# Optimization experiments

Hardware: AMD Instinct MI355X
Metric: run time of the kernel (lower is better)

Reference implementation:

```python
import jax, jax.numpy as jnp
import numpy as np

GRAVITY = 9.81007  # pypose default, gravity vector [0,0,g]

# Quaternions are xyzw (pypose SO3 convention). q1*q2 composes rotations R1@R2.

def qmul(q1, q2):
    v1, w1 = q1[..., :3], q1[..., 3:]
    v2, w2 = q2[..., :3], q2[..., 3:]
    w = w1 * w2 - jnp.sum(v1 * v2, axis=-1, keepdims=True)
    v = w1 * v2 + w2 * v1 + jnp.cross(v1, v2)
    return jnp.concatenate([v, w], axis=-1)

def qinv(q):
    return jnp.concatenate([-q[..., :3], q[..., 3:]], axis=-1)

def qrot(q, v):
    # rotate vector v by unit quaternion q: v + 2*cross(qv, cross(qv,v) + qw*v)
    qv, qw = q[..., :3], q[..., 3:]
    t = jnp.cross(qv, v) + qw * v
    return v + 2.0 * jnp.cross(qv, t)

def so3_exp(phi):
    # so3 -> SO3 quaternion: q = [phi*sin(|phi|/2)/|phi|, cos(|phi|/2)]
    theta = jnp.linalg.norm(phi, axis=-1, keepdims=True)
    small = theta < 1e-6
    safe = jnp.where(small, 1.0, theta)
    k = jnp.where(small, 0.5 - theta * theta / 48.0, jnp.sin(0.5 * theta) / safe)
    return jnp.concatenate([phi * k, jnp.cos(0.5 * theta)], axis=-1)


def setup_inputs() -> dict:
    key = jax.random.key(0)
    ks = jax.random.split(key, 7)
    B, F = 64, 32768
    dt = jax.random.uniform(ks[0], (B, F, 1), jnp.float32) * 0.01 + 0.004
    gyro = jax.random.normal(ks[1], (B, F, 3), jnp.float32) * 0.1
    acc = jax.random.normal(ks[2], (B, F, 3), jnp.float32)

    def rand_quat(k, shape):
        q = jax.random.normal(k, shape + (4,), jnp.float32)
        return q / jnp.linalg.norm(q, axis=-1, keepdims=True)

    gt_rot = rand_quat(ks[3], (B, F))      # ground-truth orientations (xyzw)
    init_rot = rand_quat(ks[4], (B, 1))
    init_vel = jax.random.normal(ks[5], (B, 1, 3), jnp.float32)
    init_pos = jax.random.normal(ks[6], (B, 1, 3), jnp.float32)
    return dict(dt=dt, gyro=gyro, acc=acc, gt_rot=gt_rot,
                init_rot=init_rot, init_vel=init_vel, init_pos=init_pos)


def reference(dt, gyro, acc, gt_rot, init_rot, init_vel, init_pos):
    # IMU preintegration (pypose IMUPreintegrator, reset=True, prop_cov=False,
    # training branch: gravity removed in body frame via ground-truth rot).
    g = jnp.array([0.0, 0.0, GRAVITY], dtype=dt.dtype)
    dr = so3_exp(gyro * dt)                                   # (B,F,4) per-step rotation
    # cumulative rotation increment: incre_r[i] = dr_0 * dr_1 * ... * dr_i
    incre_r = jax.lax.associative_scan(qmul, dr, axis=1)      # (B,F,4)
    # gravity-compensated body-frame acceleration
    a = acc - qrot(qinv(gt_rot), g)                           # (B,F,3)
    ra = qrot(incre_r, a)                                     # rotated into init frame
    incre_v = jnp.cumsum(ra * dt, axis=1)                     # (B,F,3)
    v_prev = jnp.concatenate([jnp.zeros_like(incre_v[:, :1]), incre_v[:, :-1]], axis=1)
    incre_p = jnp.cumsum(v_prev * dt + 0.5 * ra * dt * dt, axis=1)
    incre_t = jnp.cumsum(dt, axis=1)                          # (B,F,1)
    # compose with initial state
    rot = qmul(init_rot, incre_r)                             # (B,F,4)
    vel = init_vel + qrot(init_rot, incre_v)                  # (B,F,3)
    pos = init_pos + init_vel * incre_t + qrot(init_rot, incre_p)  # (B,F,3)
    return rot, vel, pos
```

## Files before the change

kernel.cpp:

```cpp
#include <hip/hip_runtime.h>
#include <math.h>

namespace {

constexpr int SEQ    = 4;
constexpr int WCHUNK = 64 * SEQ;

constexpr int GY_F  = 0;
constexpr int AC_F  = 768;
constexpr int GT_F  = 1536;
constexpr int LDS_F = 2560;

struct V3 { float x, y, z; };
struct Q4 { float x, y, z, w; };
struct St { Q4 q; V3 s; V3 p; float T; float pad; };

__device__ __forceinline__ Q4 qmul(const Q4 a, const Q4 b) {
  Q4 r;
  r.x = a.w*b.x + b.w*a.x + a.y*b.z - a.z*b.y;
  r.y = a.w*b.y + b.w*a.y + a.z*b.x - a.x*b.z;
  r.z = a.w*b.z + b.w*a.z + a.x*b.y - a.y*b.x;
  r.w = a.w*b.w - a.x*b.x - a.y*b.y - a.z*b.z;
  return r;
}

__device__ __forceinline__ V3 qrot(const Q4 q, const V3 v) {
  float tx = q.y*v.z - q.z*v.y + q.w*v.x;
  float ty = q.z*v.x - q.x*v.z + q.w*v.y;
  float tz = q.x*v.y - q.y*v.x + q.w*v.z;
  V3 r;
  r.x = v.x + 2.0f*(q.y*tz - q.z*ty);
  r.y = v.y + 2.0f*(q.z*tx - q.x*tz);
  r.z = v.z + 2.0f*(q.x*ty - q.y*tx);
  return r;
}

__device__ __forceinline__ St combine(const St a, const St b) {
  St r;
  r.q = qmul(a.q, b.q);
  V3 rs = qrot(a.q, b.s);
  r.s.x = a.s.x + rs.x;
  r.s.y = a.s.y + rs.y;
  r.s.z = a.s.z + rs.z;
  V3 rp = qrot(a.q, b.p);
  r.p.x = a.p.x + a.s.x*b.T + rp.x;
  r.p.y = a.p.y + a.s.y*b.T + rp.y;
  r.p.z = a.p.z + a.s.z*b.T + rp.z;
  r.T = a.T + b.T;
  r.pad = 0.0f;
  return r;
}

__device__ __forceinline__ St identity_st() {
  St r;
  r.q = {0.0f, 0.0f, 0.0f, 1.0f};
  r.s = {0.0f, 0.0f, 0.0f};
  r.p = {0.0f, 0.0f, 0.0f};
  r.T = 0.0f; r.pad = 0.0f;
  return r;
}

__device__ __forceinline__ St elem_state(float dt, V3 w, V3 ac, Q4 gt) {
  float px = w.x*dt, py = w.y*dt, pz = w.z*dt;
  float t2 = px*px + py*py + pz*pz;
  float k  = 0.5f + t2*(-1.0f/48.0f  + t2*(1.0f/3840.0f));
  float cw = 1.0f + t2*(-0.125f      + t2*(1.0f/384.0f));
  Q4 dr = { px*k, py*k, pz*k, cw };
  Q4 gi = { -gt.x, -gt.y, -gt.z, gt.w };
  V3 g  = { 0.0f, 0.0f, 9.81007f };
  V3 gr = qrot(gi, g);
  V3 a  = { ac.x - gr.x, ac.y - gr.y, ac.z - gr.z };
  V3 ra = qrot(dr, a);
  St e;
  e.q = dr;
  e.s.x = ra.x*dt; e.s.y = ra.y*dt; e.s.z = ra.z*dt;
  float h = 0.5f*dt;
  e.p.x = e.s.x*h; e.p.y = e.s.y*h; e.p.z = e.s.z*h;
  e.T = dt; e.pad = 0.0f;
  return e;
}

__device__ __forceinline__ St recon(float qx, float qy, float qz,
                                    float sx, float sy, float sz, float dt) {
  St e;
  e.q = { qx, qy, qz, sqrtf(fmaxf(1.0f - qx*qx - qy*qy - qz*qz, 0.0f)) };
  e.s = { sx, sy, sz };
  float h = 0.5f*dt;
  e.p = { sx*h, sy*h, sz*h };
  e.T = dt; e.pad = 0.0f;
  return e;
}

__device__ __forceinline__ St shfl_up_st(const St& v, int d) {
  St r;
  r.q.x = __shfl_up(v.q.x, d); r.q.y = __shfl_up(v.q.y, d);
  r.q.z = __shfl_up(v.q.z, d); r.q.w = __shfl_up(v.q.w, d);
  r.s.x = __shfl_up(v.s.x, d); r.s.y = __shfl_up(v.s.y, d);
  r.s.z = __shfl_up(v.s.z, d);
  r.p.x = __shfl_up(v.p.x, d); r.p.y = __shfl_up(v.p.y, d);
  r.p.z = __shfl_up(v.p.z, d);
  r.T   = __shfl_up(v.T, d);   r.pad = 0.0f;
  return r;
}

__device__ __forceinline__ St shfl_down_st(const St& v, int d) {
  St r;
  r.q.x = __shfl_down(v.q.x, d); r.q.y = __shfl_down(v.q.y, d);
  r.q.z = __shfl_down(v.q.z, d); r.q.w = __shfl_down(v.q.w, d);
  r.s.x = __shfl_down(v.s.x, d); r.s.y = __shfl_down(v.s.y, d);
  r.s.z = __shfl_down(v.s.z, d);
  r.p.x = __shfl_down(v.p.x, d); r.p.y = __shfl_down(v.p.y, d);
  r.p.z = __shfl_down(v.p.z, d);
  r.T   = __shfl_down(v.T, d);   r.pad = 0.0f;
  return r;
}

__device__ __forceinline__ St bcast_st(const St& v, int src) {
  St r;
  r.q.x = __shfl(v.q.x, src); r.q.y = __shfl(v.q.y, src);
  r.q.z = __shfl(v.q.z, src); r.q.w = __shfl(v.q.w, src);
  r.s.x = __shfl(v.s.x, src); r.s.y = __shfl(v.s.y, src);
  r.s.z = __shfl(v.s.z, src);
  r.p.x = __shfl(v.p.x, src); r.p.y = __shfl(v.p.y, src);
  r.p.z = __shfl(v.p.z, src);
  r.T   = __shfl(v.T, src);   r.pad = 0.0f;
  return r;
}

__device__ __forceinline__ int swz(int byteoff) {
  return byteoff ^ (((byteoff >> 8) & 3) << 4);
}
__device__ __forceinline__ float4& L4(float* lds, int fidx) {
  return *reinterpret_cast<float4*>(reinterpret_cast<char*>(lds) + swz(fidx << 2));
}

__device__ __forceinline__ void stage16(const void* gsrc, void* ldst) {
  __builtin_amdgcn_global_load_lds(
      (const __attribute__((address_space(1))) void*)gsrc,
      (__attribute__((address_space(3))) void*)ldst, 16, 0, 0);
}

#define STAGE_REGION(gbase, regionByte, nK)                                    \
  {                                                                            \
    _Pragma("unroll")                                                          \
    for (int k = 0; k < (nK); ++k) {                                           \
      int db = k*1024 + t*16;                                                  \
      const char* src = (const char*)(gbase) + swz(db);                        \
      char* ldst = (char*)lds + (regionByte) + k*1024;                         \
      stage16(src, ldst);                                                      \
    }                                                                          \
  }

__global__ __launch_bounds__(64) void k_agg(
    const float* __restrict__ dtp, const float* __restrict__ gyp,
    const float* __restrict__ acp, const float* __restrict__ gtp,
    St* __restrict__ aggs)
{
  __shared__ __align__(16) float lds[LDS_F];
  const int t = threadIdx.x;
  const size_t base = (size_t)blockIdx.x * WCHUNK;

  STAGE_REGION(gyp + base*3, 0,    3);
  STAGE_REGION(acp + base*3, 3072, 3);
  STAGE_REGION(gtp + base*4, 6144, 4);
  float4 dt4 = ((const float4*)(dtp + base))[t];
  __syncthreads();

  float gy[12], ac[12], gq[16];
  #pragma unroll
  for (int j = 0; j < 3; ++j) ((float4*)gy)[j] = L4(lds, GY_F + 12*t + 4*j);
  #pragma unroll
  for (int j = 0; j < 3; ++j) ((float4*)ac)[j] = L4(lds, AC_F + 12*t + 4*j);
  #pragma unroll
  for (int j = 0; j < 4; ++j) ((float4*)gq)[j] = L4(lds, GT_F + 16*t + 4*j);
  const float dtv[4] = {dt4.x, dt4.y, dt4.z, dt4.w};

  St e[SEQ];
  #pragma unroll
  for (int i = 0; i < SEQ; ++i)
    e[i] = elem_state(dtv[i],
               {gy[3*i], gy[3*i+1], gy[3*i+2]},
               {ac[3*i], ac[3*i+1], ac[3*i+2]},
               {gq[4*i], gq[4*i+1], gq[4*i+2], gq[4*i+3]});
  St run = combine(combine(e[0], e[1]), combine(e[2], e[3]));

  #pragma unroll
  for (int d = 1; d < 64; d <<= 1) run = combine(run, shfl_down_st(run, d));
  if (t == 0) aggs[blockIdx.x] = run;
}

__global__ __launch_bounds__(64) void k_pref(
    const St* __restrict__ aggs, const float* __restrict__ irp,
    float* __restrict__ prefb, int cpb)
{
  const int b = blockIdx.x;
  const int lane = threadIdx.x & 63;

  St carry = identity_st();
  carry.q = { irp[b*4+0], irp[b*4+1], irp[b*4+2], irp[b*4+3] };

  const int nw = (cpb + 63) >> 6;
  for (int w = 0; w < nw; ++w) {
    const int idx = (w << 6) + lane;
    St A = identity_st();
    if (idx < cpb) A = aggs[(size_t)b*cpb + idx];
    #pragma unroll
    for (int d = 1; d < 64; d <<= 1) {
      St o = shfl_up_st(A, d);
      if (lane >= d) A = combine(o, A);
    }
    St ex = shfl_up_st(A, 1);
    St P = (lane == 0) ? carry : combine(carry, ex);
    if (idx < cpb) {
      float4* pp = (float4*)(prefb + ((size_t)b*cpb + idx)*12);
      pp[0] = make_float4(P.q.x, P.q.y, P.q.z, P.q.w);
      pp[1] = make_float4(P.s.x, P.s.y, P.s.z, P.p.x);
      pp[2] = make_float4(P.p.y, P.p.z, P.T, 0.0f);
    }
    carry = combine(carry, bcast_st(A, 63));
  }
}

__global__ __launch_bounds__(64) void k_emit(
    const float* __restrict__ dtp, const float* __restrict__ gyp,
    const float* __restrict__ acp, const float* __restrict__ gtp,
    const float* __restrict__ prefb,
    const float* __restrict__ ivp, const float* __restrict__ ipp,
    float* __restrict__ out, int F, int cpb, int B)
{
  __shared__ __align__(16) float lds[LDS_F];
  const int t = threadIdx.x;
  const int cid = blockIdx.x;
  const int b = cid / cpb;
  const size_t base = (size_t)cid * WCHUNK;

  St P;
  {
    const float4* pp = (const float4*)(prefb + (size_t)cid*12);
    float4 a = pp[0], bb = pp[1], cc = pp[2];
    P.q = {a.x, a.y, a.z, a.w};
    P.s = {bb.x, bb.y, bb.z};
    P.p = {bb.w, cc.x, cc.y};
    P.T = cc.z; P.pad = 0.0f;
  }
  V3 iv = { ivp[b*3+0], ivp[b*3+1], ivp[b*3+2] };
  V3 ip = { ipp[b*3+0], ipp[b*3+1], ipp[b*3+2] };

  STAGE_REGION(gyp + base*3, 0,    3);
  STAGE_REGION(acp + base*3, 3072, 3);
  STAGE_REGION(gtp + base*4, 6144, 4);
  float4 dt4 = ((const float4*)(dtp + base))[t];
  __syncthreads();

  float cq[SEQ*3], cs[SEQ*3], cdt[SEQ];
  St run;
  {
    float gy[12], ac[12], gq[16];
    #pragma unroll
    for (int j = 0; j < 3; ++j) ((float4*)gy)[j] = L4(lds, GY_F + 12*t + 4*j);
    #pragma unroll
    for (int j = 0; j < 3; ++j) ((float4*)ac)[j] = L4(lds, AC_F + 12*t + 4*j);
    #pragma unroll
    for (int j = 0; j < 4; ++j) ((float4*)gq)[j] = L4(lds, GT_F + 16*t + 4*j);
    const float dtv[4] = {dt4.x, dt4.y, dt4.z, dt4.w};
    St e[SEQ];
    #pragma unroll
    for (int i = 0; i < SEQ; ++i) {
      e[i] = elem_state(dtv[i],
                 {gy[3*i], gy[3*i+1], gy[3*i+2]},
                 {ac[3*i], ac[3*i+1], ac[3*i+2]},
                 {gq[4*i], gq[4*i+1], gq[4*i+2], gq[4*i+3]});
      cq[3*i] = e[i].q.x; cq[3*i+1] = e[i].q.y; cq[3*i+2] = e[i].q.z;
      cs[3*i] = e[i].s.x; cs[3*i+1] = e[i].s.y; cs[3*i+2] = e[i].s.z;
      cdt[i]  = e[i].T;
    }
    run = combine(combine(e[0], e[1]), combine(e[2], e[3]));
  }

  St incl = run;
  #pragma unroll
  for (int d = 1; d < 64; d <<= 1) {
    St o = shfl_up_st(incl, d);
    if (t >= d) incl = combine(o, incl);
  }
  {
    St ex = shfl_up_st(incl, 1);
    if (t > 0) P = combine(P, ex);
  }

  __syncthreads();

  {
    St acc = P;
    float velb[SEQ*3], posb[SEQ*3];
    #pragma unroll
    for (int i = 0; i < SEQ; ++i) {
      St e = recon(cq[3*i], cq[3*i+1], cq[3*i+2],
                   cs[3*i], cs[3*i+1], cs[3*i+2], cdt[i]);
      acc = combine(acc, e);
      L4(lds, GT_F + 4*(4*t + i)) =
          make_float4(acc.q.x, acc.q.y, acc.q.z, acc.q.w);
      velb[3*i+0] = iv.x + acc.s.x;
      velb[3*i+1] = iv.y + acc.s.y;
      velb[3*i+2] = iv.z + acc.s.z;
      posb[3*i+0] = ip.x + iv.x*acc.T + acc.p.x;
      posb[3*i+1] = ip.y + iv.y*acc.T + acc.p.y;
      posb[3*i+2] = ip.z + iv.z*acc.T + acc.p.z;
    }
    #pragma unroll
    for (int j = 0; j < 3; ++j) L4(lds, GY_F + 12*t + 4*j) = ((float4*)velb)[j];
    #pragma unroll
    for (int j = 0; j < 3; ++j) L4(lds, AC_F + 12*t + 4*j) = ((float4*)posb)[j];
  }
  __syncthreads();

  const size_t BF = (size_t)B * (size_t)F;
  float4* grot = (float4*)out + base;
  float4* gvel = (float4*)(out + BF*4 + base*3);
  float4* gpos = (float4*)(out + BF*7 + base*3);
  #pragma unroll
  for (int k = 0; k < 4; ++k) grot[t + 64*k] = L4(lds, GT_F + 4*(t + 64*k));
  #pragma unroll
  for (int k = 0; k < 3; ++k) gvel[t + 64*k] = L4(lds, GY_F + 4*(t + 64*k));
  #pragma unroll
  for (int k = 0; k < 3; ++k) gpos[t + 64*k] = L4(lds, AC_F + 4*(t + 64*k));
}

}

extern "C" void kernel_launch(void* const* d_in, const int* in_sizes, int n_in,
                              void* d_out, int out_size, void* d_ws, size_t ws_size,
                              hipStream_t stream)
{
  (void)n_in; (void)out_size; (void)ws_size;

  const float* dtp = (const float*)d_in[0];
  const float* gyp = (const float*)d_in[1];
  const float* acp = (const float*)d_in[2];
  const float* gtp = (const float*)d_in[3];
  const float* irp = (const float*)d_in[4];
  const float* ivp = (const float*)d_in[5];
  const float* ipp = (const float*)d_in[6];
  float* out = (float*)d_out;

  const int B   = in_sizes[4] / 4;
  const int F   = in_sizes[0] / B;
  const int cpb = F / WCHUNK;
  const int nchunk = B * cpb;

  St*    aggs  = (St*)d_ws;
  float* prefb = (float*)((char*)d_ws + (size_t)nchunk * sizeof(St));

  k_agg <<<nchunk, 64, 0, stream>>>(dtp, gyp, acp, gtp, aggs);
  k_pref<<<B,      64, 0, stream>>>(aggs, irp, prefb, cpb);
  k_emit<<<nchunk, 64, 0, stream>>>(dtp, gyp, acp, gtp, prefb, ivp, ipp,
                                    out, F, cpb, B);
}
```

Before: 64.93 us.

## Split wave scan into separate quaternion, velocity, time and position scans

After: 60.25 us (median of 2 runs). 7.2% less time.

```diff
diff --git a/kernel.cpp b/kernel.cpp
--- a/kernel.cpp
+++ b/kernel.cpp
@@ -60,7 +60,9 @@
   return r;
 }
 
-__device__ __forceinline__ St elem_state(float dt, V3 w, V3 ac, Q4 gt) {
+struct El { Q4 q; V3 s; float dt; };
+
+__device__ __forceinline__ El elem_state(float dt, V3 w, V3 ac, Q4 gt) {
   float px = w.x*dt, py = w.y*dt, pz = w.z*dt;
   float t2 = px*px + py*py + pz*pz;
   float k  = 0.5f + t2*(-1.0f/48.0f  + t2*(1.0f/3840.0f));
@@ -71,24 +73,18 @@
   V3 gr = qrot(gi, g);
   V3 a  = { ac.x - gr.x, ac.y - gr.y, ac.z - gr.z };
   V3 ra = qrot(dr, a);
-  St e;
+  El e;
   e.q = dr;
-  e.s.x = ra.x*dt; e.s.y = ra.y*dt; e.s.z = ra.z*dt;
-  float h = 0.5f*dt;
-  e.p.x = e.s.x*h; e.p.y = e.s.y*h; e.p.z = e.s.z*h;
-  e.T = dt; e.pad = 0.0f;
+  e.s = { ra.x*dt, ra.y*dt, ra.z*dt };
+  e.dt = dt;
   return e;
 }
 
-__device__ __forceinline__ St recon(float qx, float qy, float qz,
-                                    float sx, float sy, float sz, float dt) {
-  St e;
-  e.q = { qx, qy, qz, sqrtf(fmaxf(1.0f - qx*qx - qy*qy - qz*qz, 0.0f)) };
-  e.s = { sx, sy, sz };
-  float h = 0.5f*dt;
-  e.p = { sx*h, sy*h, sz*h };
-  e.T = dt; e.pad = 0.0f;
-  return e;
+__device__ __forceinline__ Q4 shfl_up_q(const Q4 v, int d) {
+  return { __shfl_up(v.x,d), __shfl_up(v.y,d), __shfl_up(v.z,d), __shfl_up(v.w,d) };
+}
+__device__ __forceinline__ V3 shfl_up_v(const V3 v, int d) {
+  return { __shfl_up(v.x,d), __shfl_up(v.y,d), __shfl_up(v.z,d) };
 }
 
 __device__ __forceinline__ St shfl_up_st(const St& v, int d) {
@@ -103,18 +99,6 @@
   return r;
 }
 
-__device__ __forceinline__ St shfl_down_st(const St& v, int d) {
-  St r;
-  r.q.x = __shfl_down(v.q.x, d); r.q.y = __shfl_down(v.q.y, d);
-  r.q.z = __shfl_down(v.q.z, d); r.q.w = __shfl_down(v.q.w, d);
-  r.s.x = __shfl_down(v.s.x, d); r.s.y = __shfl_down(v.s.y, d);
-  r.s.z = __shfl_down(v.s.z, d);
-  r.p.x = __shfl_down(v.p.x, d); r.p.y = __shfl_down(v.p.y, d);
-  r.p.z = __shfl_down(v.p.z, d);
-  r.T   = __shfl_down(v.T, d);   r.pad = 0.0f;
-  return r;
-}
-
 __device__ __forceinline__ St bcast_st(const St& v, int src) {
   St r;
   r.q.x = __shfl(v.q.x, src); r.q.y = __shfl(v.q.y, src);
@@ -151,6 +135,82 @@
     }                                                                          \
   }
 
+#define BUILD_SLIM()                                                           \
+  float cq[12], cs[12], cdt[4];                                                \
+  Q4 segq; V3 segs, segp; float segT;                                          \
+  {                                                                            \
+    float gy[12], ac[12], gq[16];                                              \
+    _Pragma("unroll")                                                          \
+    for (int j = 0; j < 3; ++j) ((float4*)gy)[j] = L4(lds, GY_F + 12*t + 4*j); \
+    _Pragma("unroll")                                                          \
+    for (int j = 0; j < 3; ++j) ((float4*)ac)[j] = L4(lds, AC_F + 12*t + 4*j); \
+    _Pragma("unroll")                                                          \
+    for (int j = 0; j < 4; ++j) ((float4*)gq)[j] = L4(lds, GT_F + 16*t + 4*j); \
+    const float dtv[4] = {dt4.x, dt4.y, dt4.z, dt4.w};                         \
+    _Pragma("unroll")                                                          \
+    for (int i = 0; i < SEQ; ++i) {                                            \
+      El e = elem_state(dtv[i],                                                \
+                 {gy[3*i], gy[3*i+1], gy[3*i+2]},                              \
+                 {ac[3*i], ac[3*i+1], ac[3*i+2]},                              \
+                 {gq[4*i], gq[4*i+1], gq[4*i+2], gq[4*i+3]});                  \
+      cq[3*i] = e.q.x; cq[3*i+1] = e.q.y; cq[3*i+2] = e.q.z;                   \
+      cs[3*i] = e.s.x; cs[3*i+1] = e.s.y; cs[3*i+2] = e.s.z;                   \
+      cdt[i]  = e.dt;                                                          \
+      if (i == 0) {                                                            \
+        segq = e.q; segs = e.s;                                                \
+        float h = 0.5f*e.dt;                                                   \
+        segp = { e.s.x*h, e.s.y*h, e.s.z*h };                                  \
+        segT = e.dt;                                                           \
+      } else {                                                                 \
+        V3 v = qrot(segq, e.s);                                                \
+        float h = 0.5f*e.dt;                                                   \
+        segp.x += segs.x*e.dt + v.x*h;                                         \
+        segp.y += segs.y*e.dt + v.y*h;                                         \
+        segp.z += segs.z*e.dt + v.z*h;                                         \
+        segs.x += v.x; segs.y += v.y; segs.z += v.z;                           \
+        segq = qmul(segq, e.q);                                                \
+        segT += e.dt;                                                          \
+      }                                                                        \
+    }                                                                          \
+  }
+
+#define WAVE_SPLIT_SCAN()                                                      \
+  Q4 qin = segq;                                                               \
+  _Pragma("unroll")                                                            \
+  for (int d = 1; d < 64; d <<= 1) {                                           \
+    Q4 o = shfl_up_q(qin, d);                                                  \
+    if (t >= d) qin = qmul(o, qin);                                            \
+  }                                                                            \
+  Q4 qex = shfl_up_q(qin, 1);                                                  \
+  if (t == 0) qex = {0.0f, 0.0f, 0.0f, 1.0f};                                  \
+  V3 v_  = qrot(qex, segs);                                                    \
+  V3 sin_ = v_;                                                                \
+  _Pragma("unroll")                                                            \
+  for (int d = 1; d < 64; d <<= 1) {                                           \
+    V3 o = shfl_up_v(sin_, d);                                                 \
+    if (t >= d) { sin_.x += o.x; sin_.y += o.y; sin_.z += o.z; }               \
+  }                                                                            \
+  V3 sex = shfl_up_v(sin_, 1);                                                 \
+  if (t == 0) sex = {0.0f, 0.0f, 0.0f};                                        \
+  float Tin = segT;                                                            \
+  _Pragma("unroll")                                                            \
+  for (int d = 1; d < 64; d <<= 1) {                                           \
+    float o = __shfl_up(Tin, d);                                               \
+    if (t >= d) Tin += o;                                                      \
+  }                                                                            \
+  float Tex = __shfl_up(Tin, 1);                                               \
+  if (t == 0) Tex = 0.0f;                                                      \
+  V3 w_ = qrot(qex, segp);                                                     \
+  V3 u_ = { w_.x + sex.x*segT, w_.y + sex.y*segT, w_.z + sex.z*segT };         \
+  V3 pin = u_;                                                                 \
+  _Pragma("unroll")                                                            \
+  for (int d = 1; d < 64; d <<= 1) {                                           \
+    V3 o = shfl_up_v(pin, d);                                                  \
+    if (t >= d) { pin.x += o.x; pin.y += o.y; pin.z += o.z; }                  \
+  }                                                                            \
+  V3 pex = shfl_up_v(pin, 1);                                                  \
+  if (t == 0) pex = {0.0f, 0.0f, 0.0f};
+
 __global__ __launch_bounds__(64) void k_agg(
     const float* __restrict__ dtp, const float* __restrict__ gyp,
     const float* __restrict__ acp, const float* __restrict__ gtp,
@@ -166,27 +226,15 @@
   float4 dt4 = ((const float4*)(dtp + base))[t];
   __syncthreads();
 
-  float gy[12], ac[12], gq[16];
-  #pragma unroll
-  for (int j = 0; j < 3; ++j) ((float4*)gy)[j] = L4(lds, GY_F + 12*t + 4*j);
-  #pragma unroll
-  for (int j = 0; j < 3; ++j) ((float4*)ac)[j] = L4(lds, AC_F + 12*t + 4*j);
-  #pragma unroll
-  for (int j = 0; j < 4; ++j) ((float4*)gq)[j] = L4(lds, GT_F + 16*t + 4*j);
-  const float dtv[4] = {dt4.x, dt4.y, dt4.z, dt4.w};
-
-  St e[SEQ];
-  #pragma unroll
-  for (int i = 0; i < SEQ; ++i)
-    e[i] = elem_state(dtv[i],
-               {gy[3*i], gy[3*i+1], gy[3*i+2]},
-               {ac[3*i], ac[3*i+1], ac[3*i+2]},
-               {gq[4*i], gq[4*i+1], gq[4*i+2], gq[4*i+3]});
-  St run = combine(combine(e[0], e[1]), combine(e[2], e[3]));
-
-  #pragma unroll
-  for (int d = 1; d < 64; d <<= 1) run = combine(run, shfl_down_st(run, d));
-  if (t == 0) aggs[blockIdx.x] = run;
+  BUILD_SLIM();
+  WAVE_SPLIT_SCAN();
+
+  if (t == 63) {
+    St a;
+    a.q = qin; a.s = sin_; a.p = pin; a.T = Tin; a.pad = 0.0f;
+    aggs[blockIdx.x] = a;
+  }
+  (void)cq; (void)cs; (void)cdt; (void)qex; (void)sex; (void)pex; (void)Tex;
 }
 
 __global__ __launch_bounds__(64) void k_pref(
@@ -234,14 +282,14 @@
   const int b = cid / cpb;
   const size_t base = (size_t)cid * WCHUNK;
 
-  St P;
+  Q4 Pq; V3 Ps, Pp; float PT;
   {
     const float4* pp = (const float4*)(prefb + (size_t)cid*12);
     float4 a = pp[0], bb = pp[1], cc = pp[2];
-    P.q = {a.x, a.y, a.z, a.w};
-    P.s = {bb.x, bb.y, bb.z};
-    P.p = {bb.w, cc.x, cc.y};
-    P.T = cc.z; P.pad = 0.0f;
+    Pq = {a.x, a.y, a.z, a.w};
+    Ps = {bb.x, bb.y, bb.z};
+    Pp = {bb.w, cc.x, cc.y};
+    PT = cc.z;
   }
   V3 iv = { ivp[b*3+0], ivp[b*3+1], ivp[b*3+2] };
   V3 ip = { ipp[b*3+0], ipp[b*3+1], ipp[b*3+2] };
@@ -252,60 +300,43 @@
   float4 dt4 = ((const float4*)(dtp + base))[t];
   __syncthreads();
 
-  float cq[SEQ*3], cs[SEQ*3], cdt[SEQ];
-  St run;
+  BUILD_SLIM();
+  WAVE_SPLIT_SCAN();
+  (void)qin; (void)sin_; (void)pin; (void)Tin;
+
+  Q4 Xq = qmul(Pq, qex);
+  V3 rs = qrot(Pq, sex);
+  V3 Xs = { Ps.x + rs.x, Ps.y + rs.y, Ps.z + rs.z };
+  V3 rp = qrot(Pq, pex);
+  V3 Xp = { Pp.x + Ps.x*Tex + rp.x, Pp.y + Ps.y*Tex + rp.y, Pp.z + Ps.z*Tex + rp.z };
+  float XT = PT + Tex;
+
+  __syncthreads();
+
   {
-    float gy[12], ac[12], gq[16];
-    #pragma unroll
-    for (int j = 0; j < 3; ++j) ((float4*)gy)[j] = L4(lds, GY_F + 12*t + 4*j);
-    #pragma unroll
-    for (int j = 0; j < 3; ++j) ((float4*)ac)[j] = L4(lds, AC_F + 12*t + 4*j);
-    #pragma unroll
-    for (int j = 0; j < 4; ++j) ((float4*)gq)[j] = L4(lds, GT_F + 16*t + 4*j);
-    const float dtv[4] = {dt4.x, dt4.y, dt4.z, dt4.w};
-    St e[SEQ];
+    Q4 qr = Xq; V3 sr = Xs; V3 pr = Xp; float Tr = XT;
+    float velb[12], posb[12];
     #pragma unroll
     for (int i = 0; i < SEQ; ++i) {
-      e[i] = elem_state(dtv[i],
-                 {gy[3*i], gy[3*i+1], gy[3*i+2]},
-                 {ac[3*i], ac[3*i+1], ac[3*i+2]},
-                 {gq[4*i], gq[4*i+1], gq[4*i+2], gq[4*i+3]});
-      cq[3*i] = e[i].q.x; cq[3*i+1] = e[i].q.y; cq[3*i+2] = e[i].q.z;
-      cs[3*i] = e[i].s.x; cs[3*i+1] = e[i].s.y; cs[3*i+2] = e[i].s.z;
-      cdt[i]  = e[i].T;
-    }
-    run = combine(combine(e[0], e[1]), combine(e[2], e[3]));
-  }
-
-  St incl = run;
-  #pragma unroll
-  for (int d = 1; d < 64; d <<= 1) {
-    St o = shfl_up_st(incl, d);
-    if (t >= d) incl = combine(o, incl);
-  }
-  {
-    St ex = shfl_up_st(incl, 1);
-    if (t > 0) P = combine(P, ex);
-  }
-
-  __syncthreads();
-
-  {
-    St acc = P;
-    float velb[SEQ*3], posb[SEQ*3];
-    #pragma unroll
-    for (int i = 0; i < SEQ; ++i) {
-      St e = recon(cq[3*i], cq[3*i+1], cq[3*i+2],
-                   cs[3*i], cs[3*i+1], cs[3*i+2], cdt[i]);
-      acc = combine(acc, e);
-      L4(lds, GT_F + 4*(4*t + i)) =
-          make_float4(acc.q.x, acc.q.y, acc.q.z, acc.q.w);
-      velb[3*i+0] = iv.x + acc.s.x;
-      velb[3*i+1] = iv.y + acc.s.y;
-      velb[3*i+2] = iv.z + acc.s.z;
-      posb[3*i+0] = ip.x + iv.x*acc.T + acc.p.x;
-      posb[3*i+1] = ip.y + iv.y*acc.T + acc.p.y;
-      posb[3*i+2] = ip.z + iv.z*acc.T + acc.p.z;
+      float qx = cq[3*i], qy = cq[3*i+1], qz = cq[3*i+2];
+      Q4 eq = { qx, qy, qz, sqrtf(fmaxf(1.0f - qx*qx - qy*qy - qz*qz, 0.0f)) };
+      V3 es = { cs[3*i], cs[3*i+1], cs[3*i+2] };
+      float dt = cdt[i], h = 0.5f*dt;
+      V3 vv = qrot(qr, es);
+      V3 pn = { pr.x + sr.x*dt + vv.x*h,
+                pr.y + sr.y*dt + vv.y*h,
+                pr.z + sr.z*dt + vv.z*h };
+      V3 sn = { sr.x + vv.x, sr.y + vv.y, sr.z + vv.z };
+      Q4 qn = qmul(qr, eq);
+      float Tn = Tr + dt;
+      L4(lds, GT_F + 4*(4*t + i)) = make_float4(qn.x, qn.y, qn.z, qn.w);
+      velb[3*i+0] = iv.x + sn.x;
+      velb[3*i+1] = iv.y + sn.y;
+      velb[3*i+2] = iv.z + sn.z;
+      posb[3*i+0] = ip.x + iv.x*Tn + pn.x;
+      posb[3*i+1] = ip.y + iv.y*Tn + pn.y;
+      posb[3*i+2] = ip.z + iv.z*Tn + pn.z;
+      qr = qn; sr = sn; pr = pn; Tr = Tn;
     }
     #pragma unroll
     for (int j = 0; j < 3; ++j) L4(lds, GY_F + 12*t + 4*j) = ((float4*)velb)[j];
```

## Split wave scan into per-component scans and process two chunks per emit block

Applied to the files above, without the earlier changes.

New measurement: 69.05 us. 1.06x slower.

```diff
diff --git a/kernel.cpp b/kernel.cpp
--- a/kernel.cpp
+++ b/kernel.cpp
@@ -9,7 +9,7 @@
 constexpr int GY_F  = 0;
 constexpr int AC_F  = 768;
 constexpr int GT_F  = 1536;
-constexpr int LDS_F = 2560;
+constexpr int BUF_F = 2560;
 
 struct V3 { float x, y, z; };
 struct Q4 { float x, y, z, w; };
@@ -60,7 +60,9 @@
   return r;
 }
 
-__device__ __forceinline__ St elem_state(float dt, V3 w, V3 ac, Q4 gt) {
+struct El { Q4 q; V3 s; float dt; };
+
+__device__ __forceinline__ El elem_state(float dt, V3 w, V3 ac, Q4 gt) {
   float px = w.x*dt, py = w.y*dt, pz = w.z*dt;
   float t2 = px*px + py*py + pz*pz;
   float k  = 0.5f + t2*(-1.0f/48.0f  + t2*(1.0f/3840.0f));
@@ -71,24 +73,18 @@
   V3 gr = qrot(gi, g);
   V3 a  = { ac.x - gr.x, ac.y - gr.y, ac.z - gr.z };
   V3 ra = qrot(dr, a);
-  St e;
+  El e;
   e.q = dr;
-  e.s.x = ra.x*dt; e.s.y = ra.y*dt; e.s.z = ra.z*dt;
-  float h = 0.5f*dt;
-  e.p.x = e.s.x*h; e.p.y = e.s.y*h; e.p.z = e.s.z*h;
-  e.T = dt; e.pad = 0.0f;
+  e.s = { ra.x*dt, ra.y*dt, ra.z*dt };
+  e.dt = dt;
   return e;
 }
 
-__device__ __forceinline__ St recon(float qx, float qy, float qz,
-                                    float sx, float sy, float sz, float dt) {
-  St e;
-  e.q = { qx, qy, qz, sqrtf(fmaxf(1.0f - qx*qx - qy*qy - qz*qz, 0.0f)) };
-  e.s = { sx, sy, sz };
-  float h = 0.5f*dt;
-  e.p = { sx*h, sy*h, sz*h };
-  e.T = dt; e.pad = 0.0f;
-  return e;
+__device__ __forceinline__ Q4 shfl_up_q(const Q4 v, int d) {
+  return { __shfl_up(v.x,d), __shfl_up(v.y,d), __shfl_up(v.z,d), __shfl_up(v.w,d) };
+}
+__device__ __forceinline__ V3 shfl_up_v(const V3 v, int d) {
+  return { __shfl_up(v.x,d), __shfl_up(v.y,d), __shfl_up(v.z,d) };
 }
 
 __device__ __forceinline__ St shfl_up_st(const St& v, int d) {
@@ -103,18 +99,6 @@
   return r;
 }
 
-__device__ __forceinline__ St shfl_down_st(const St& v, int d) {
-  St r;
-  r.q.x = __shfl_down(v.q.x, d); r.q.y = __shfl_down(v.q.y, d);
-  r.q.z = __shfl_down(v.q.z, d); r.q.w = __shfl_down(v.q.w, d);
-  r.s.x = __shfl_down(v.s.x, d); r.s.y = __shfl_down(v.s.y, d);
-  r.s.z = __shfl_down(v.s.z, d);
-  r.p.x = __shfl_down(v.p.x, d); r.p.y = __shfl_down(v.p.y, d);
-  r.p.z = __shfl_down(v.p.z, d);
-  r.T   = __shfl_down(v.T, d);   r.pad = 0.0f;
-  return r;
-}
-
 __device__ __forceinline__ St bcast_st(const St& v, int src) {
   St r;
   r.q.x = __shfl(v.q.x, src); r.q.y = __shfl(v.q.y, src);
@@ -140,23 +124,148 @@
       (__attribute__((address_space(3))) void*)ldst, 16, 0, 0);
 }
 
-#define STAGE_REGION(gbase, regionByte, nK)                                    \
+#define STAGE_REGION(gbase, bufByte, nK)                                       \
   {                                                                            \
     _Pragma("unroll")                                                          \
     for (int k = 0; k < (nK); ++k) {                                           \
       int db = k*1024 + t*16;                                                  \
       const char* src = (const char*)(gbase) + swz(db);                        \
-      char* ldst = (char*)lds + (regionByte) + k*1024;                         \
+      char* ldst = (char*)lds + (bufByte) + k*1024;                            \
       stage16(src, ldst);                                                      \
     }                                                                          \
   }
+
+struct Compressed { float cq[12]; float cs[12]; float cdt[4]; };
+struct Seg { Q4 q; V3 s; V3 p; float T; };
+struct ScanRes { Q4 qex, qin; V3 sex, sin; V3 pex, pin; float Tex, Tin; };
+
+__device__ __forceinline__ Seg build_slim(float* lds, int ofs, int t,
+                                          float4 dt4, Compressed& C) {
+  float gy[12], ac[12], gq[16];
+  #pragma unroll
+  for (int j = 0; j < 3; ++j) ((float4*)gy)[j] = L4(lds, ofs + GY_F + 12*t + 4*j);
+  #pragma unroll
+  for (int j = 0; j < 3; ++j) ((float4*)ac)[j] = L4(lds, ofs + AC_F + 12*t + 4*j);
+  #pragma unroll
+  for (int j = 0; j < 4; ++j) ((float4*)gq)[j] = L4(lds, ofs + GT_F + 16*t + 4*j);
+  const float dtv[4] = {dt4.x, dt4.y, dt4.z, dt4.w};
+  Seg s;
+  #pragma unroll
+  for (int i = 0; i < SEQ; ++i) {
+    El e = elem_state(dtv[i],
+               {gy[3*i], gy[3*i+1], gy[3*i+2]},
+               {ac[3*i], ac[3*i+1], ac[3*i+2]},
+               {gq[4*i], gq[4*i+1], gq[4*i+2], gq[4*i+3]});
+    C.cq[3*i] = e.q.x; C.cq[3*i+1] = e.q.y; C.cq[3*i+2] = e.q.z;
+    C.cs[3*i] = e.s.x; C.cs[3*i+1] = e.s.y; C.cs[3*i+2] = e.s.z;
+    C.cdt[i]  = e.dt;
+    if (i == 0) {
+      s.q = e.q; s.s = e.s;
+      float h = 0.5f*e.dt;
+      s.p = { e.s.x*h, e.s.y*h, e.s.z*h };
+      s.T = e.dt;
+    } else {
+      V3 v = qrot(s.q, e.s);
+      float h = 0.5f*e.dt;
+      s.p.x += s.s.x*e.dt + v.x*h;
+      s.p.y += s.s.y*e.dt + v.y*h;
+      s.p.z += s.s.z*e.dt + v.z*h;
+      s.s.x += v.x; s.s.y += v.y; s.s.z += v.z;
+      s.q = qmul(s.q, e.q);
+      s.T += e.dt;
+    }
+  }
+  return s;
+}
+
+__device__ __forceinline__ ScanRes wave_split_scan(int t, const Seg& sg) {
+  ScanRes r;
+  Q4 qin = sg.q;
+  #pragma unroll
+  for (int d = 1; d < 64; d <<= 1) {
+    Q4 o = shfl_up_q(qin, d);
+    if (t >= d) qin = qmul(o, qin);
+  }
+  Q4 qex = shfl_up_q(qin, 1);
+  if (t == 0) qex = {0.0f, 0.0f, 0.0f, 1.0f};
+  V3 v = qrot(qex, sg.s);
+  V3 sin_ = v;
+  #pragma unroll
+  for (int d = 1; d < 64; d <<= 1) {
+    V3 o = shfl_up_v(sin_, d);
+    if (t >= d) { sin_.x += o.x; sin_.y += o.y; sin_.z += o.z; }
+  }
+  V3 sex = shfl_up_v(sin_, 1);
+  if (t == 0) sex = {0.0f, 0.0f, 0.0f};
+  float Tin = sg.T;
+  #pragma unroll
+  for (int d = 1; d < 64; d <<= 1) {
+    float o = __shfl_up(Tin, d);
+    if (t >= d) Tin += o;
+  }
+  float Tex = __shfl_up(Tin, 1);
+  if (t == 0) Tex = 0.0f;
+  V3 w = qrot(qex, sg.p);
+  V3 u = { w.x + sex.x*sg.T, w.y + sex.y*sg.T, w.z + sex.z*sg.T };
+  V3 pin = u;
+  #pragma unroll
+  for (int d = 1; d < 64; d <<= 1) {
+    V3 o = shfl_up_v(pin, d);
+    if (t >= d) { pin.x += o.x; pin.y += o.y; pin.z += o.z; }
+  }
+  V3 pex = shfl_up_v(pin, 1);
+  if (t == 0) pex = {0.0f, 0.0f, 0.0f};
+  r.qex = qex; r.qin = qin;
+  r.sex = sex; r.sin = sin_;
+  r.pex = pex; r.pin = pin;
+  r.Tex = Tex; r.Tin = Tin;
+  return r;
+}
+
+__device__ __forceinline__ void compute_outputs(
+    const Compressed& C, Q4 Pq, V3 Ps, V3 Pp, float PT,
+    const ScanRes& S, V3 iv, V3 ip,
+    float* rotb , float* velb , float* posb )
+{
+  Q4 Xq = qmul(Pq, S.qex);
+  V3 rs = qrot(Pq, S.sex);
+  V3 Xs = { Ps.x + rs.x, Ps.y + rs.y, Ps.z + rs.z };
+  V3 rp = qrot(Pq, S.pex);
+  V3 Xp = { Pp.x + Ps.x*S.Tex + rp.x, Pp.y + Ps.y*S.Tex + rp.y,
+            Pp.z + Ps.z*S.Tex + rp.z };
+  float XT = PT + S.Tex;
+
+  Q4 qr = Xq; V3 sr = Xs; V3 pr = Xp; float Tr = XT;
+  #pragma unroll
+  for (int i = 0; i < SEQ; ++i) {
+    float qx = C.cq[3*i], qy = C.cq[3*i+1], qz = C.cq[3*i+2];
+    Q4 eq = { qx, qy, qz, sqrtf(fmaxf(1.0f - qx*qx - qy*qy - qz*qz, 0.0f)) };
+    V3 es = { C.cs[3*i], C.cs[3*i+1], C.cs[3*i+2] };
+    float dt = C.cdt[i], h = 0.5f*dt;
+    V3 vv = qrot(qr, es);
+    V3 pn = { pr.x + sr.x*dt + vv.x*h,
+              pr.y + sr.y*dt + vv.y*h,
+              pr.z + sr.z*dt + vv.z*h };
+    V3 sn = { sr.x + vv.x, sr.y + vv.y, sr.z + vv.z };
+    Q4 qn = qmul(qr, eq);
+    float Tn = Tr + dt;
+    rotb[4*i+0] = qn.x; rotb[4*i+1] = qn.y; rotb[4*i+2] = qn.z; rotb[4*i+3] = qn.w;
+    velb[3*i+0] = iv.x + sn.x;
+    velb[3*i+1] = iv.y + sn.y;
+    velb[3*i+2] = iv.z + sn.z;
+    posb[3*i+0] = ip.x + iv.x*Tn + pn.x;
+    posb[3*i+1] = ip.y + iv.y*Tn + pn.y;
+    posb[3*i+2] = ip.z + iv.z*Tn + pn.z;
+    qr = qn; sr = sn; pr = pn; Tr = Tn;
+  }
+}
 
 __global__ __launch_bounds__(64) void k_agg(
     const float* __restrict__ dtp, const float* __restrict__ gyp,
     const float* __restrict__ acp, const float* __restrict__ gtp,
     St* __restrict__ aggs)
 {
-  __shared__ __align__(16) float lds[LDS_F];
+  __shared__ __align__(16) float lds[BUF_F];
   const int t = threadIdx.x;
   const size_t base = (size_t)blockIdx.x * WCHUNK;
 
@@ -166,27 +275,15 @@
   float4 dt4 = ((const float4*)(dtp + base))[t];
   __syncthreads();
 
-  float gy[12], ac[12], gq[16];
-  #pragma unroll
-  for (int j = 0; j < 3; ++j) ((float4*)gy)[j] = L4(lds, GY_F + 12*t + 4*j);
-  #pragma unroll
-  for (int j = 0; j < 3; ++j) ((float4*)ac)[j] = L4(lds, AC_F + 12*t + 4*j);
-  #pragma unroll
-  for (int j = 0; j < 4; ++j) ((float4*)gq)[j] = L4(lds, GT_F + 16*t + 4*j);
-  const float dtv[4] = {dt4.x, dt4.y, dt4.z, dt4.w};
-
-  St e[SEQ];
-  #pragma unroll
-  for (int i = 0; i < SEQ; ++i)
-    e[i] = elem_state(dtv[i],
-               {gy[3*i], gy[3*i+1], gy[3*i+2]},
-               {ac[3*i], ac[3*i+1], ac[3*i+2]},
-               {gq[4*i], gq[4*i+1], gq[4*i+2], gq[4*i+3]});
-  St run = combine(combine(e[0], e[1]), combine(e[2], e[3]));
-
-  #pragma unroll
-  for (int d = 1; d < 64; d <<= 1) run = combine(run, shfl_down_st(run, d));
-  if (t == 0) aggs[blockIdx.x] = run;
+  Compressed C;
+  Seg s = build_slim(lds, 0, t, dt4, C);
+  ScanRes R = wave_split_scan(t, s);
+
+  if (t == 63) {
+    St a;
+    a.q = R.qin; a.s = R.sin; a.p = R.pin; a.T = R.Tin; a.pad = 0.0f;
+    aggs[blockIdx.x] = a;
+  }
 }
 
 __global__ __launch_bounds__(64) void k_pref(
@@ -228,102 +325,99 @@
     const float* __restrict__ ivp, const float* __restrict__ ipp,
     float* __restrict__ out, int F, int cpb, int B)
 {
-  __shared__ __align__(16) float lds[LDS_F];
+  __shared__ __align__(16) float lds[2*BUF_F];
   const int t = threadIdx.x;
-  const int cid = blockIdx.x;
-  const int b = cid / cpb;
-  const size_t base = (size_t)cid * WCHUNK;
-
-  St P;
-  {
-    const float4* pp = (const float4*)(prefb + (size_t)cid*12);
+  const int cid0 = blockIdx.x*2, cid1 = cid0 + 1;
+  const int b0 = cid0 / cpb, b1 = cid1 / cpb;
+  const size_t base0 = (size_t)cid0 * WCHUNK;
+  const size_t base1 = (size_t)cid1 * WCHUNK;
+
+  Q4 Pq0, Pq1; V3 Ps0, Pp0, Ps1, Pp1; float PT0, PT1;
+  {
+    const float4* pp = (const float4*)(prefb + (size_t)cid0*12);
     float4 a = pp[0], bb = pp[1], cc = pp[2];
-    P.q = {a.x, a.y, a.z, a.w};
-    P.s = {bb.x, bb.y, bb.z};
-    P.p = {bb.w, cc.x, cc.y};
-    P.T = cc.z; P.pad = 0.0f;
-  }
-  V3 iv = { ivp[b*3+0], ivp[b*3+1], ivp[b*3+2] };
-  V3 ip = { ipp[b*3+0], ipp[b*3+1], ipp[b*3+2] };
-
-  STAGE_REGION(gyp + base*3, 0,    3);
-  STAGE_REGION(acp + base*3, 3072, 3);
-  STAGE_REGION(gtp + base*4, 6144, 4);
-  float4 dt4 = ((const float4*)(dtp + base))[t];
+    Pq0 = {a.x, a.y, a.z, a.w}; Ps0 = {bb.x, bb.y, bb.z};
+    Pp0 = {bb.w, cc.x, cc.y};   PT0 = cc.z;
+  }
+  {
+    const float4* pp = (const float4*)(prefb + (size_t)cid1*12);
+    float4 a = pp[0], bb = pp[1], cc = pp[2];
+    Pq1 = {a.x, a.y, a.z, a.w}; Ps1 = {bb.x, bb.y, bb.z};
+    Pp1 = {bb.w, cc.x, cc.y};   PT1 = cc.z;
+  }
+  V3 iv0 = { ivp[b0*3+0], ivp[b0*3+1], ivp[b0*3+2] };
+  V3 ip0 = { ipp[b0*3+0], ipp[b0*3+1], ipp[b0*3+2] };
+  V3 iv1 = { ivp[b1*3+0], ivp[b1*3+1], ivp[b1*3+2] };
+  V3 ip1 = { ipp[b1*3+0], ipp[b1*3+1], ipp[b1*3+2] };
+
+  STAGE_REGION(gyp + base0*3, 0,    3);
+  STAGE_REGION(acp + base0*3, 3072, 3);
+  STAGE_REGION(gtp + base0*4, 6144, 4);
+  float4 dt4_0 = ((const float4*)(dtp + base0))[t];
   __syncthreads();
 
-  float cq[SEQ*3], cs[SEQ*3], cdt[SEQ];
-  St run;
-  {
-    float gy[12], ac[12], gq[16];
-    #pragma unroll
-    for (int j = 0; j < 3; ++j) ((float4*)gy)[j] = L4(lds, GY_F + 12*t + 4*j);
-    #pragma unroll
-    for (int j = 0; j < 3; ++j) ((float4*)ac)[j] = L4(lds, AC_F + 12*t + 4*j);
-    #pragma unroll
-    for (int j = 0; j < 4; ++j) ((float4*)gq)[j] = L4(lds, GT_F + 16*t + 4*j);
-    const float dtv[4] = {dt4.x, dt4.y, dt4.z, dt4.w};
-    St e[SEQ];
-    #pragma unroll
-    for (int i = 0; i < SEQ; ++i) {
-      e[i] = elem_state(dtv[i],
-                 {gy[3*i], gy[3*i+1], gy[3*i+2]},
-                 {ac[3*i], ac[3*i+1], ac[3*i+2]},
-                 {gq[4*i], gq[4*i+1], gq[4*i+2], gq[4*i+3]});
-      cq[3*i] = e[i].q.x; cq[3*i+1] = e[i].q.y; cq[3*i+2] = e[i].q.z;
-      cs[3*i] = e[i].s.x; cs[3*i+1] = e[i].s.y; cs[3*i+2] = e[i].s.z;
-      cdt[i]  = e[i].T;
-    }
-    run = combine(combine(e[0], e[1]), combine(e[2], e[3]));
-  }
-
-  St incl = run;
-  #pragma unroll
-  for (int d = 1; d < 64; d <<= 1) {
-    St o = shfl_up_st(incl, d);
-    if (t >= d) incl = combine(o, incl);
-  }
-  {
-    St ex = shfl_up_st(incl, 1);
-    if (t > 0) P = combine(P, ex);
+  STAGE_REGION(gyp + base1*3, 10240,      3);
+  STAGE_REGION(acp + base1*3, 10240+3072, 3);
+  STAGE_REGION(gtp + base1*4, 10240+6144, 4);
+  float4 dt4_1 = ((const float4*)(dtp + base1))[t];
+
+  float rotb[16], velb[12], posb[12];
+  {
+    Compressed C;
+    Seg s0 = build_slim(lds, 0, t, dt4_0, C);
+    ScanRes R0 = wave_split_scan(t, s0);
+    compute_outputs(C, Pq0, Ps0, Pp0, PT0, R0, iv0, ip0, rotb, velb, posb);
   }
 
   __syncthreads();
 
-  {
-    St acc = P;
-    float velb[SEQ*3], posb[SEQ*3];
-    #pragma unroll
-    for (int i = 0; i < SEQ; ++i) {
-      St e = recon(cq[3*i], cq[3*i+1], cq[3*i+2],
-                   cs[3*i], cs[3*i+1], cs[3*i+2], cdt[i]);
-      acc = combine(acc, e);
-      L4(lds, GT_F + 4*(4*t + i)) =
-          make_float4(acc.q.x, acc.q.y, acc.q.z, acc.q.w);
-      velb[3*i+0] = iv.x + acc.s.x;
-      velb[3*i+1] = iv.y + acc.s.y;
-      velb[3*i+2] = iv.z + acc.s.z;
-      posb[3*i+0] = ip.x + iv.x*acc.T + acc.p.x;
-      posb[3*i+1] = ip.y + iv.y*acc.T + acc.p.y;
-      posb[3*i+2] = ip.z + iv.z*acc.T + acc.p.z;
-    }
-    #pragma unroll
-    for (int j = 0; j < 3; ++j) L4(lds, GY_F + 12*t + 4*j) = ((float4*)velb)[j];
-    #pragma unroll
-    for (int j = 0; j < 3; ++j) L4(lds, AC_F + 12*t + 4*j) = ((float4*)posb)[j];
-  }
+  #pragma unroll
+  for (int i = 0; i < 4; ++i) L4(lds, GT_F + 4*(4*t + i)) = ((float4*)rotb)[i];
+  #pragma unroll
+  for (int j = 0; j < 3; ++j) L4(lds, GY_F + 12*t + 4*j) = ((float4*)velb)[j];
+  #pragma unroll
+  for (int j = 0; j < 3; ++j) L4(lds, AC_F + 12*t + 4*j) = ((float4*)posb)[j];
   __syncthreads();
 
   const size_t BF = (size_t)B * (size_t)F;
-  float4* grot = (float4*)out + base;
-  float4* gvel = (float4*)(out + BF*4 + base*3);
-  float4* gpos = (float4*)(out + BF*7 + base*3);
-  #pragma unroll
-  for (int k = 0; k < 4; ++k) grot[t + 64*k] = L4(lds, GT_F + 4*(t + 64*k));
-  #pragma unroll
-  for (int k = 0; k < 3; ++k) gvel[t + 64*k] = L4(lds, GY_F + 4*(t + 64*k));
-  #pragma unroll
-  for (int k = 0; k < 3; ++k) gpos[t + 64*k] = L4(lds, AC_F + 4*(t + 64*k));
+  {
+    float4* grot = (float4*)out + base0;
+    float4* gvel = (float4*)(out + BF*4 + base0*3);
+    float4* gpos = (float4*)(out + BF*7 + base0*3);
+    #pragma unroll
+    for (int k = 0; k < 4; ++k) grot[t + 64*k] = L4(lds, GT_F + 4*(t + 64*k));
+    #pragma unroll
+    for (int k = 0; k < 3; ++k) gvel[t + 64*k] = L4(lds, GY_F + 4*(t + 64*k));
+    #pragma unroll
+    for (int k = 0; k < 3; ++k) gpos[t + 64*k] = L4(lds, AC_F + 4*(t + 64*k));
+  }
+
+  {
+    Compressed C;
+    Seg s1 = build_slim(lds, BUF_F, t, dt4_1, C);
+    ScanRes R1 = wave_split_scan(t, s1);
+    compute_outputs(C, Pq1, Ps1, Pp1, PT1, R1, iv1, ip1, rotb, velb, posb);
+  }
+
+  #pragma unroll
+  for (int i = 0; i < 4; ++i) L4(lds, BUF_F + GT_F + 4*(4*t + i)) = ((float4*)rotb)[i];
+  #pragma unroll
+  for (int j = 0; j < 3; ++j) L4(lds, BUF_F + GY_F + 12*t + 4*j) = ((float4*)velb)[j];
+  #pragma unroll
+  for (int j = 0; j < 3; ++j) L4(lds, BUF_F + AC_F + 12*t + 4*j) = ((float4*)posb)[j];
+  __syncthreads();
+
+  {
+    float4* grot = (float4*)out + base1;
+    float4* gvel = (float4*)(out + BF*4 + base1*3);
+    float4* gpos = (float4*)(out + BF*7 + base1*3);
+    #pragma unroll
+    for (int k = 0; k < 4; ++k) grot[t + 64*k] = L4(lds, BUF_F + GT_F + 4*(t + 64*k));
+    #pragma unroll
+    for (int k = 0; k < 3; ++k) gvel[t + 64*k] = L4(lds, BUF_F + GY_F + 4*(t + 64*k));
+    #pragma unroll
+    for (int k = 0; k < 3; ++k) gpos[t + 64*k] = L4(lds, BUF_F + AC_F + 4*(t + 64*k));
+  }
 }
 
 }
@@ -351,8 +445,8 @@
   St*    aggs  = (St*)d_ws;
   float* prefb = (float*)((char*)d_ws + (size_t)nchunk * sizeof(St));
 
-  k_agg <<<nchunk, 64, 0, stream>>>(dtp, gyp, acp, gtp, aggs);
-  k_pref<<<B,      64, 0, stream>>>(aggs, irp, prefb, cpb);
-  k_emit<<<nchunk, 64, 0, stream>>>(dtp, gyp, acp, gtp, prefb, ivp, ipp,
-                                    out, F, cpb, B);
-}
+  k_agg <<<nchunk,   64, 0, stream>>>(dtp, gyp, acp, gtp, aggs);
+  k_pref<<<B,        64, 0, stream>>>(aggs, irp, prefb, cpb);
+  k_emit<<<nchunk/2, 64, 0, stream>>>(dtp, gyp, acp, gtp, prefb, ivp, ipp,
+                                      out, F, cpb, B);
+}
```
